# Kernel tuning notes

Measured on AMD Instinct MI355X. Metric: run time of the kernel, lower is better.

The kernel has to match this reference:

```python
import jax, jax.numpy as jnp
import numpy as np

NUM_CLASSES = 80        # dataset_train.num_classes() global in the original
NUM_SUPPORT_IMAGES = 5  # classification_batch[:5*num_anchors] in the original
ALPHA, GAMMA = 0.25, 2.0
STD = jnp.array([0.1, 0.1, 0.2, 0.2], dtype=jnp.float32)


def setup_inputs() -> dict:
    key = jax.random.key(0)
    k1, k2 = jax.random.split(key)
    n, tile = 320, 4.0
    A = n * n              # 102400 anchors
    B, G, z = 8, 16, 64
    gy, gx = jnp.meshgrid(jnp.arange(n, dtype=jnp.float32),
                          jnp.arange(n, dtype=jnp.float32), indexing='ij')
    x0 = gx.reshape(-1) * tile
    y0 = gy.reshape(-1) * tile
    anchor = jnp.stack([x0, y0, x0 + tile, y0 + tile], axis=1)  # [A,4] disjoint tiles
    anchors = anchor[None]                                       # [1,A,4]
    # GT boxes exactly equal distinct anchor tiles -> IoU 1 at match, 0 elsewhere.
    jj = jnp.arange(B)[:, None]
    gg = jnp.arange(G)[None, :]
    idx = (jj * 997 + gg * 3001) % A                             # distinct per image
    boxes = anchor[idx]                                          # [B,G,4]
    labels = jnp.broadcast_to((gg % 3).astype(jnp.float32), (B, G))
    annotations = jnp.concatenate([boxes, labels[..., None]], axis=-1)  # [B,G,5]
    classifications = jax.random.normal(k1, (B, A, z), dtype=jnp.float32)
    regressions = jax.random.normal(k2, (B, A, 4), dtype=jnp.float32)
    return {"classifications": classifications, "regressions": regressions,
            "anchors": anchors, "annotations": annotations}


def reference(classifications, regressions, anchors, annotations):
    B, A, z = classifications.shape
    anchor = anchors[0]                                   # [A,4]
    aw = anchor[:, 2] - anchor[:, 0]
    ah = anchor[:, 3] - anchor[:, 1]
    acx = anchor[:, 0] + 0.5 * aw
    acy = anchor[:, 1] + 0.5 * ah

    boxes = annotations[..., :4]                          # [B,G,4] (all valid, label != -1)
    labels = annotations[..., 4]                          # [B,G]

    # pairwise IoU  [B,A,G]  (calc_iou, vectorized over batch)
    area = (boxes[..., 2] - boxes[..., 0]) * (boxes[..., 3] - boxes[..., 1])  # [B,G]
    iw = jnp.minimum(anchor[None, :, None, 2], boxes[:, None, :, 2]) - \
         jnp.maximum(anchor[None, :, None, 0], boxes[:, None, :, 0])
    ih = jnp.minimum(anchor[None, :, None, 3], boxes[:, None, :, 3]) - \
         jnp.maximum(anchor[None, :, None, 1], boxes[:, None, :, 1])
    iw = jnp.maximum(iw, 0.0)
    ih = jnp.maximum(ih, 0.0)
    inter = iw * ih
    ua = jnp.maximum((aw * ah)[None, :, None] + area[:, None, :] - inter, 1e-8)
    iou = inter / ua
    iou_max = iou.max(axis=2)                             # [B,A]
    iou_arg = iou.argmax(axis=2)                          # [B,A]

    bidx = jnp.arange(B)[:, None]
    assigned_boxes = boxes[bidx, iou_arg]                 # [B,A,4]
    assigned_labels = labels[bidx, iou_arg]               # [B,A]

    pos = iou_max >= 0.5                                  # [B,A]
    targets_cls = jnp.where(iou_max < 0.4, float(NUM_CLASSES), -1.0)
    targets_cls = jnp.where(pos, assigned_labels, targets_cls)

    rgw = assigned_boxes[..., 2] - assigned_boxes[..., 0]
    rgh = assigned_boxes[..., 3] - assigned_boxes[..., 1]
    gcx = assigned_boxes[..., 0] + 0.5 * rgw              # centers use un-clamped w/h
    gcy = assigned_boxes[..., 1] + 0.5 * rgh
    gw = jnp.maximum(rgw, 1.0)
    gh = jnp.maximum(rgh, 1.0)
    tdx = (gcx - acx[None, :]) / aw[None, :]
    tdy = (gcy - acy[None, :]) / ah[None, :]
    tdw = jnp.log(gw / aw[None, :])
    tdh = jnp.log(gh / ah[None, :])
    t = jnp.stack([tdx, tdy, tdw, tdh], axis=-1) / STD    # [B,A,4]
    diff = jnp.abs(t - regressions)
    sl1 = jnp.where(diff <= 1.0 / 9.0, 0.5 * 9.0 * diff * diff, diff - 0.5 / 9.0)
    posf = pos.astype(sl1.dtype)
    npos = posf.sum(axis=1)                               # [B]
    reg_per_img = jnp.where(npos > 0,
                            (sl1 * posf[..., None]).sum(axis=(1, 2)) / jnp.maximum(4.0 * npos, 1.0),
                            0.0)
    reg_loss = reg_per_img.mean(keepdims=True)            # shape [1]

    # ---- prototypical focal classification loss ----
    emb = classifications.reshape(B * A, z)
    tgt = targets_cls.reshape(B * A)
    ns = NUM_SUPPORT_IMAGES * A
    emb_s, lab_s = emb[:ns], tgt[:ns]
    emb_q, lab_q = emb[ns:], tgt[ns:]
    valid = lab_q != -1.0                                 # query rows with assigned target

    # unique(labels_support) -- fixed {0,1,2,80} by input construction (assert len==4)
    classes = jnp.array([0.0, 1.0, 2.0, float(NUM_CLASSES)], dtype=emb.dtype)
    onehot = (lab_s[None, :] == classes[:, None]).astype(emb.dtype)   # [4,Ns]
    proto = (onehot @ emb_s) / jnp.maximum(onehot.sum(1, keepdims=True), 1.0)  # [4,z]

    dists = ((emb_q[:, None, :] - proto[None, :, :]) ** 2).sum(-1)    # [Nq,4]
    p_y = jax.nn.softmax(-dists, axis=1)
    tidx = jnp.clip(jnp.searchsorted(classes, lab_q), 0, classes.shape[0] - 1)
    prob = jnp.take_along_axis(p_y, tidx[:, None], axis=1)[:, 0]
    cls_term = -ALPHA * (1.0 - prob) ** GAMMA * jnp.log(prob)
    cls_term = jnp.where(valid, cls_term, 0.0)
    npq = (valid & (lab_q != float(NUM_CLASSES))).sum().astype(cls_term.dtype)
    cls_loss = cls_term.sum() / jnp.maximum(npq, 1.0)

    return cls_loss, reg_loss
```

## Files before the change

kernel.cpp:

```cpp
#include <hip/hip_runtime.h>

#define NB 8
#define NA 102400
#define NGRID 320
#define NG 16
#define NSUP 5
#define NQ 3
#define NCLSF 80.0f
#define NSLICE 8
#define SLS 264
#define WS_REG   (NSLICE * SLS)
#define WS_NPOS  (WS_REG + NB)
#define WS_CLS   (WS_NPOS + NB)
#define WS_NPQ   (WS_CLS + 4)
#define WS_FLOATS (WS_NPQ + 4)
#define BPI 400

__device__ __forceinline__ void anchor_of(int a, float& ax0, float& ay0,
                                          float& ax1, float& ay1) {
    int i = a / NGRID;
    int j = a - i * NGRID;
    ax0 = (float)j * 4.0f;
    ay0 = (float)i * 4.0f;
    ax1 = ax0 + 4.0f;
    ay1 = ay0 + 4.0f;
}

__device__ __forceinline__ void assign_anchor(const float* ann, int a,
                                              float& tgt, int& arg, float& iou_max) {
    float ax0, ay0, ax1, ay1;
    anchor_of(a, ax0, ay0, ax1, ay1);
    float aw = ax1 - ax0, ah = ay1 - ay0;
    float aarea = aw * ah;
    float best = -1.0f;
    int bi = 0;
    #pragma unroll
    for (int j = 0; j < NG; ++j) {
        float bx0 = ann[j * 5 + 0], by0 = ann[j * 5 + 1];
        float bx1 = ann[j * 5 + 2], by1 = ann[j * 5 + 3];
        float iw = fmaxf(fminf(ax1, bx1) - fmaxf(ax0, bx0), 0.0f);
        float ih = fmaxf(fminf(ay1, by1) - fmaxf(ay0, by0), 0.0f);
        float inter = iw * ih;
        float area = (bx1 - bx0) * (by1 - by0);
        float ua = fmaxf(aarea + area - inter, 1e-8f);
        float iou = inter / ua;
        if (iou > best) { best = iou; bi = j; }
    }
    iou_max = best;
    arg = bi;
    float lab = ann[bi * 5 + 4];
    tgt = (best >= 0.5f) ? lab : ((best < 0.4f) ? NCLSF : -1.0f);
}

__device__ __forceinline__ int code_of(float tgt) {
    int vld = (tgt != -1.0f) ? 4 : 0;
    int tix = (tgt == NCLSF) ? 3 : ((tgt == 2.0f) ? 2 : ((tgt == 1.0f) ? 1 : 0));
    return tix | vld;
}

__device__ __forceinline__ void reg_partial(const float* ann, int a, int arg, float im,
                                            const float* __restrict__ regressions,
                                            size_t row, float& sl1, float& posf) {
    sl1 = 0.0f; posf = 0.0f;
    if (im >= 0.5f) {
        posf = 1.0f;
        float ax0, ay0, ax1, ay1;
        anchor_of(a, ax0, ay0, ax1, ay1);
        float aw = ax1 - ax0, ah = ay1 - ay0;
        float acx = ax0 + 0.5f * aw, acy = ay0 + 0.5f * ah;
        const float* bb = ann + arg * 5;
        float rgw = bb[2] - bb[0], rgh = bb[3] - bb[1];
        float gcx = bb[0] + 0.5f * rgw, gcy = bb[1] + 0.5f * rgh;
        float gw = fmaxf(rgw, 1.0f), gh = fmaxf(rgh, 1.0f);
        float t0 = ((gcx - acx) / aw) / 0.1f;
        float t1 = ((gcy - acy) / ah) / 0.1f;
        float t2 = logf(gw / aw) / 0.2f;
        float t3 = logf(gh / ah) / 0.2f;
        const float4 rg4 = *reinterpret_cast<const float4*>(regressions + row * 4);
        float d0 = fabsf(t0 - rg4.x), d1 = fabsf(t1 - rg4.y);
        float d2 = fabsf(t2 - rg4.z), d3 = fabsf(t3 - rg4.w);
        sl1 += (d0 <= (1.0f/9.0f)) ? (4.5f * d0 * d0) : (d0 - 0.5f/9.0f);
        sl1 += (d1 <= (1.0f/9.0f)) ? (4.5f * d1 * d1) : (d1 - 0.5f/9.0f);
        sl1 += (d2 <= (1.0f/9.0f)) ? (4.5f * d2 * d2) : (d2 - 0.5f/9.0f);
        sl1 += (d3 <= (1.0f/9.0f)) ? (4.5f * d3 * d3) : (d3 - 0.5f/9.0f);
    }
}

__global__ __launch_bounds__(256, 3) void fl_proto(const float* __restrict__ annotations,
                                                   const float* __restrict__ cls,
                                                   const float* __restrict__ regressions,
                                                   float* __restrict__ ws) {
    __shared__ float s_ann[NG * 5];
    __shared__ float s_acc[256];
    __shared__ float s_sl1[4], s_np[4];
    __shared__ int   s_cnt[4];
    int b    = blockIdx.x / BPI;
    int cb   = blockIdx.x - b * BPI;
    int wid  = threadIdx.x >> 6;
    int lane = threadIdx.x & 63;
    int rg   = lane >> 4, li = lane & 15, zi = li * 4;
    int chunk = cb * 4 + wid;
    size_t row0 = (size_t)b * NA + (size_t)chunk * 64;

    float4 v[16];
    const float4* P = (const float4*)cls + (row0 + rg) * 16 + li;
    #pragma unroll
    for (int i = 0; i < 16; ++i) v[i] = P[(size_t)i * 64];

    if (threadIdx.x < NG * 5) s_ann[threadIdx.x] = annotations[b * NG * 5 + threadIdx.x];
    s_acc[threadIdx.x] = 0.0f;
    if (threadIdx.x < 4) s_cnt[threadIdx.x] = 0;
    __syncthreads();

    int a = chunk * 64 + lane;
    float tgt; int arg; float im;
    assign_anchor(s_ann, a, tgt, arg, im);
    int ci = code_of(tgt);

    float sl1, posf;
    reg_partial(s_ann, a, arg, im, regressions, row0 + lane, sl1, posf);
    #pragma unroll
    for (int s = 1; s < 64; s <<= 1) {
        sl1  += __shfl_xor(sl1, s, 64);
        posf += __shfl_xor(posf, s, 64);
    }
    if (lane == 0) { s_sl1[wid] = sl1; s_np[wid] = posf; }

    #pragma unroll
    for (int c = 0; c < 4; ++c) {
        unsigned long long m = __ballot(ci == (c | 4));
        if (lane == 0) atomicAdd(&s_cnt[c], (int)__popcll(m));
    }

    float acc[4][4] = {};
    #pragma unroll
    for (int i = 0; i < 16; ++i) {
        int cq = __shfl(ci, 4 * i + rg, 64);
        #pragma unroll
        for (int c = 0; c < 4; ++c) {
            float sel = (cq == (c | 4)) ? 1.0f : 0.0f;
            acc[c][0] = fmaf(sel, v[i].x, acc[c][0]);
            acc[c][1] = fmaf(sel, v[i].y, acc[c][1]);
            acc[c][2] = fmaf(sel, v[i].z, acc[c][2]);
            acc[c][3] = fmaf(sel, v[i].w, acc[c][3]);
        }
    }
    #pragma unroll
    for (int c = 0; c < 4; ++c) {
        #pragma unroll
        for (int k = 0; k < 4; ++k) {
            float vv = acc[c][k];
            vv += __shfl_xor(vv, 16, 64);
            vv += __shfl_xor(vv, 32, 64);
            if (lane < 16) atomicAdd(&s_acc[c * 64 + zi + k], vv);
        }
    }
    __syncthreads();
    int slice = blockIdx.x & (NSLICE - 1);
    atomicAdd(&ws[slice * SLS + threadIdx.x], s_acc[threadIdx.x]);
    if (threadIdx.x < 4 && s_cnt[threadIdx.x] > 0)
        atomicAdd(&ws[slice * SLS + 256 + threadIdx.x], (float)s_cnt[threadIdx.x]);
    if (threadIdx.x == 0) {
        atomicAdd(&ws[WS_REG + b],  s_sl1[0] + s_sl1[1] + s_sl1[2] + s_sl1[3]);
        atomicAdd(&ws[WS_NPOS + b], s_np[0] + s_np[1] + s_np[2] + s_np[3]);
    }
}

__global__ __launch_bounds__(256, 3) void fl_query(const float* __restrict__ annotations,
                                                   const float* __restrict__ cls,
                                                   const float* __restrict__ regressions,
                                                   float* __restrict__ ws) {
    __shared__ float s_ann[NG * 5];
    __shared__ float s_cls[4], s_npq[4], s_sl1[4], s_np[4];
    int qb   = blockIdx.x / BPI;
    int b    = NSUP + qb;
    int cb   = blockIdx.x - qb * BPI;
    int wid  = threadIdx.x >> 6;
    int lane = threadIdx.x & 63;
    int rg   = lane >> 4, li = lane & 15, zi = li * 4;
    int chunk = cb * 4 + wid;
    size_t row0 = (size_t)b * NA + (size_t)chunk * 64;

    float4 v[16];
    const float4* P = (const float4*)cls + (row0 + rg) * 16 + li;
    #pragma unroll
    for (int i = 0; i < 16; ++i) v[i] = P[(size_t)i * 64];

    if (threadIdx.x < NG * 5) s_ann[threadIdx.x] = annotations[b * NG * 5 + threadIdx.x];
    __syncthreads();

    float p[4][4], q[4];
    #pragma unroll
    for (int c = 0; c < 4; ++c) {
        float cv = 0.0f, s0 = 0.0f, s1 = 0.0f, s2 = 0.0f, s3 = 0.0f;
        #pragma unroll
        for (int s = 0; s < NSLICE; ++s) {
            cv += ws[s * SLS + 256 + c];
            const float4 u = *reinterpret_cast<const float4*>(&ws[s * SLS + c * 64 + zi]);
            s0 += u.x; s1 += u.y; s2 += u.z; s3 += u.w;
        }
        cv = fmaxf(cv, 1.0f);
        p[c][0] = s0 / cv; p[c][1] = s1 / cv; p[c][2] = s2 / cv; p[c][3] = s3 / cv;
        float qp = p[c][0]*p[c][0] + p[c][1]*p[c][1] + p[c][2]*p[c][2] + p[c][3]*p[c][3];
        qp += __shfl_xor(qp, 1, 64);
        qp += __shfl_xor(qp, 2, 64);
        qp += __shfl_xor(qp, 4, 64);
        qp += __shfl_xor(qp, 8, 64);
        q[c] = qp;
    }

    int a = chunk * 64 + lane;
    float tgt; int arg; float im;
    assign_anchor(s_ann, a, tgt, arg, im);
    int code = code_of(tgt);
    float sl1, posf;
    reg_partial(s_ann, a, arg, im, regressions, row0 + lane, sl1, posf);

    float clsAcc = 0.0f, npqAcc = 0.0f;
    #pragma unroll
    for (int i = 0; i < 16; ++i) {
        int cq = __shfl(code, 4 * i + rg, 64);
        float d0 = v[i].x*p[0][0] + v[i].y*p[0][1] + v[i].z*p[0][2] + v[i].w*p[0][3];
        float d1 = v[i].x*p[1][0] + v[i].y*p[1][1] + v[i].z*p[1][2] + v[i].w*p[1][3];
        float d2 = v[i].x*p[2][0] + v[i].y*p[2][1] + v[i].z*p[2][2] + v[i].w*p[2][3];
        float d3 = v[i].x*p[3][0] + v[i].y*p[3][1] + v[i].z*p[3][2] + v[i].w*p[3][3];
        #pragma unroll
        for (int s = 1; s < 16; s <<= 1) {
            d0 += __shfl_xor(d0, s, 64);
            d1 += __shfl_xor(d1, s, 64);
            d2 += __shfl_xor(d2, s, 64);
            d3 += __shfl_xor(d3, s, 64);
        }
        float l0 = 2.0f * d0 - q[0];
        float l1 = 2.0f * d1 - q[1];
        float l2 = 2.0f * d2 - q[2];
        float l3 = 2.0f * d3 - q[3];
        float m = fmaxf(fmaxf(l0, l1), fmaxf(l2, l3));
        float ex0 = expf(l0 - m), ex1 = expf(l1 - m);
        float ex2 = expf(l2 - m), ex3 = expf(l3 - m);
        float ssum = ex0 + ex1 + ex2 + ex3;
        int tq = cq & 3;
        float pnum = (tq == 0) ? ex0 : (tq == 1) ? ex1 : (tq == 2) ? ex2 : ex3;
        float prob = pnum / ssum;
        float om = 1.0f - prob;
        float term = -0.25f * om * om * logf(prob);
        if (li == 0 && (cq & 4)) {
            clsAcc += term;
            if (tq != 3) npqAcc += 1.0f;
        }
    }

    #pragma unroll
    for (int s = 1; s < 64; s <<= 1) {
        clsAcc += __shfl_xor(clsAcc, s, 64);
        npqAcc += __shfl_xor(npqAcc, s, 64);
        sl1    += __shfl_xor(sl1, s, 64);
        posf   += __shfl_xor(posf, s, 64);
    }
    if (lane == 0) { s_cls[wid] = clsAcc; s_npq[wid] = npqAcc; s_sl1[wid] = sl1; s_np[wid] = posf; }
    __syncthreads();
    if (threadIdx.x == 0) {
        int slice = blockIdx.x & 3;
        atomicAdd(&ws[WS_CLS + slice], s_cls[0] + s_cls[1] + s_cls[2] + s_cls[3]);
        atomicAdd(&ws[WS_NPQ + slice], s_npq[0] + s_npq[1] + s_npq[2] + s_npq[3]);
        atomicAdd(&ws[WS_REG + b],  s_sl1[0] + s_sl1[1] + s_sl1[2] + s_sl1[3]);
        atomicAdd(&ws[WS_NPOS + b], s_np[0] + s_np[1] + s_np[2] + s_np[3]);
    }
}

__global__ void fl_final(const float* __restrict__ ws, float* __restrict__ out) {
    if (threadIdx.x == 0 && blockIdx.x == 0) {
        float cs = ws[WS_CLS] + ws[WS_CLS+1] + ws[WS_CLS+2] + ws[WS_CLS+3];
        float nq = ws[WS_NPQ] + ws[WS_NPQ+1] + ws[WS_NPQ+2] + ws[WS_NPQ+3];
        float clsl = cs / fmaxf(nq, 1.0f);
        float rs = 0.0f;
        #pragma unroll
        for (int b = 0; b < NB; ++b) {
            float np_ = ws[WS_NPOS + b];
            float sv  = ws[WS_REG + b];
            rs += (np_ > 0.0f) ? (sv / fmaxf(4.0f * np_, 1.0f)) : 0.0f;
        }
        out[0] = clsl;
        out[1] = rs * 0.125f;
    }
}

extern "C" void kernel_launch(void* const* d_in, const int* in_sizes, int n_in,
                              void* d_out, int out_size, void* d_ws, size_t ws_size,
                              hipStream_t stream) {
    const float* classifications = (const float*)d_in[0];
    const float* regressions    = (const float*)d_in[1];
    const float* annotations    = (const float*)d_in[3];
    float* ws  = (float*)d_ws;
    float* out = (float*)d_out;

    hipMemsetAsync(d_ws, 0, WS_FLOATS * sizeof(float), stream);
    fl_proto<<<NSUP * BPI, 256, 0, stream>>>(annotations, classifications, regressions, ws);
    fl_query<<<NQ * BPI, 256, 0, stream>>>(annotations, classifications, regressions, ws);
    fl_final<<<1, 64, 0, stream>>>(ws, out);
}
```

Baseline: 127.1 us.

## Fuse proto, query and final kernels into one persistent kernel with grid barrier

```diff
diff --git a/kernel.cpp b/kernel.cpp
--- a/kernel.cpp
+++ b/kernel.cpp
@@ -13,8 +13,9 @@
 #define WS_NPOS  (WS_REG + NB)
 #define WS_CLS   (WS_NPOS + NB)
 #define WS_NPQ   (WS_CLS + 4)
-#define WS_FLOATS (WS_NPQ + 4)
-#define BPI 400
+#define WS_CNT   (WS_NPQ + 4)
+#define WS_FLOATS (WS_CNT + 2)
+#define NBLK 512
 
 __device__ __forceinline__ void anchor_of(int a, float& ax0, float& ay0,
                                           float& ax1, float& ay1) {
@@ -61,9 +62,8 @@
 __device__ __forceinline__ void reg_partial(const float* ann, int a, int arg, float im,
                                             const float* __restrict__ regressions,
                                             size_t row, float& sl1, float& posf) {
-    sl1 = 0.0f; posf = 0.0f;
     if (im >= 0.5f) {
-        posf = 1.0f;
+        posf += 1.0f;
         float ax0, ay0, ax1, ay1;
         anchor_of(a, ax0, ay0, ax1, ay1);
         float aw = ax1 - ax0, ah = ay1 - ay0;
@@ -86,108 +86,125 @@
     }
 }
 
-__global__ __launch_bounds__(256, 3) void fl_proto(const float* __restrict__ annotations,
+__global__ __launch_bounds__(256, 2) void fl_fused(const float* __restrict__ annotations,
                                                    const float* __restrict__ cls,
                                                    const float* __restrict__ regressions,
-                                                   float* __restrict__ ws) {
-    __shared__ float s_ann[NG * 5];
+                                                   float* __restrict__ ws,
+                                                   float* __restrict__ out) {
+    const int tid  = threadIdx.x;
+    const int lane = tid & 63, wid = tid >> 6;
+    const int gw   = blockIdx.x * 4 + wid;
+    const int rg   = lane >> 4, li = lane & 15, zi = li * 4;
+    unsigned* cnt = (unsigned*)(ws + WS_CNT);
+
     __shared__ float s_acc[256];
-    __shared__ float s_sl1[4], s_np[4];
-    __shared__ int   s_cnt[4];
-    int b    = blockIdx.x / BPI;
-    int cb   = blockIdx.x - b * BPI;
-    int wid  = threadIdx.x >> 6;
-    int lane = threadIdx.x & 63;
-    int rg   = lane >> 4, li = lane & 15, zi = li * 4;
-    int chunk = cb * 4 + wid;
-    size_t row0 = (size_t)b * NA + (size_t)chunk * 64;
-
-    float4 v[16];
-    const float4* P = (const float4*)cls + (row0 + rg) * 16 + li;
-    #pragma unroll
-    for (int i = 0; i < 16; ++i) v[i] = P[(size_t)i * 64];
-
-    if (threadIdx.x < NG * 5) s_ann[threadIdx.x] = annotations[b * NG * 5 + threadIdx.x];
-    s_acc[threadIdx.x] = 0.0f;
-    if (threadIdx.x < 4) s_cnt[threadIdx.x] = 0;
-    __syncthreads();
-
-    int a = chunk * 64 + lane;
-    float tgt; int arg; float im;
-    assign_anchor(s_ann, a, tgt, arg, im);
-    int ci = code_of(tgt);
-
-    float sl1, posf;
-    reg_partial(s_ann, a, arg, im, regressions, row0 + lane, sl1, posf);
+    __shared__ float s_cnt[4];
+    __shared__ float s_red[4][4];
+
+    s_acc[tid] = 0.0f;
+    if (tid < 4) s_cnt[tid] = 0.0f;
+    __syncthreads();
+
+    float sl1 = 0.0f, posf = 0.0f;
+    if (gw < 2000) {
+        const int b = gw / 400;
+        const float* ann = annotations + b * NG * 5;
+        float acc[4][4] = {};
+        float cc0 = 0.0f, cc1 = 0.0f, cc2 = 0.0f, cc3 = 0.0f;
+        for (int k = 0; k < 4; ++k) {
+            const int g   = gw * 4 + k;
+            const int cii = g - b * 1600;
+            const size_t row0 = (size_t)b * NA + (size_t)cii * 64;
+            const float4* P = (const float4*)cls + (row0 + rg) * 16 + li;
+            float4 v0[8];
+            #pragma unroll
+            for (int i = 0; i < 8; ++i) v0[i] = P[(size_t)i * 64];
+            const int a = cii * 64 + lane;
+            float tgt; int arg; float im;
+            assign_anchor(ann, a, tgt, arg, im);
+            const int ci = code_of(tgt);
+            reg_partial(ann, a, arg, im, regressions, row0 + lane, sl1, posf);
+            float4 v1[8];
+            #pragma unroll
+            for (int i = 0; i < 8; ++i) v1[i] = P[(size_t)(i + 8) * 64];
+            #pragma unroll
+            for (int i = 0; i < 8; ++i) {
+                const int cq = __shfl(ci, 4 * i + rg, 64);
+                #pragma unroll
+                for (int c = 0; c < 4; ++c) {
+                    const float sel = (cq == (c | 4)) ? 1.0f : 0.0f;
+                    acc[c][0] = fmaf(sel, v0[i].x, acc[c][0]);
+                    acc[c][1] = fmaf(sel, v0[i].y, acc[c][1]);
+                    acc[c][2] = fmaf(sel, v0[i].z, acc[c][2]);
+                    acc[c][3] = fmaf(sel, v0[i].w, acc[c][3]);
+                }
+            }
+            #pragma unroll
+            for (int i = 0; i < 8; ++i) {
+                const int cq = __shfl(ci, 4 * (i + 8) + rg, 64);
+                #pragma unroll
+                for (int c = 0; c < 4; ++c) {
+                    const float sel = (cq == (c | 4)) ? 1.0f : 0.0f;
+                    acc[c][0] = fmaf(sel, v1[i].x, acc[c][0]);
+                    acc[c][1] = fmaf(sel, v1[i].y, acc[c][1]);
+                    acc[c][2] = fmaf(sel, v1[i].z, acc[c][2]);
+                    acc[c][3] = fmaf(sel, v1[i].w, acc[c][3]);
+                }
+            }
+            cc0 += (float)__popcll(__ballot(ci == (0 | 4)));
+            cc1 += (float)__popcll(__ballot(ci == (1 | 4)));
+            cc2 += (float)__popcll(__ballot(ci == (2 | 4)));
+            cc3 += (float)__popcll(__ballot(ci == (3 | 4)));
+        }
+        #pragma unroll
+        for (int c = 0; c < 4; ++c) {
+            #pragma unroll
+            for (int k = 0; k < 4; ++k) {
+                float vv = acc[c][k];
+                vv += __shfl_xor(vv, 16, 64);
+                vv += __shfl_xor(vv, 32, 64);
+                if (lane < 16) atomicAdd(&s_acc[c * 64 + zi + k], vv);
+            }
+        }
+        if (lane == 0) {
+            atomicAdd(&s_cnt[0], cc0);
+            atomicAdd(&s_cnt[1], cc1);
+            atomicAdd(&s_cnt[2], cc2);
+            atomicAdd(&s_cnt[3], cc3);
+        }
+    }
     #pragma unroll
     for (int s = 1; s < 64; s <<= 1) {
         sl1  += __shfl_xor(sl1, s, 64);
         posf += __shfl_xor(posf, s, 64);
     }
-    if (lane == 0) { s_sl1[wid] = sl1; s_np[wid] = posf; }
-
-    #pragma unroll
-    for (int c = 0; c < 4; ++c) {
-        unsigned long long m = __ballot(ci == (c | 4));
-        if (lane == 0) atomicAdd(&s_cnt[c], (int)__popcll(m));
-    }
-
-    float acc[4][4] = {};
-    #pragma unroll
-    for (int i = 0; i < 16; ++i) {
-        int cq = __shfl(ci, 4 * i + rg, 64);
-        #pragma unroll
-        for (int c = 0; c < 4; ++c) {
-            float sel = (cq == (c | 4)) ? 1.0f : 0.0f;
-            acc[c][0] = fmaf(sel, v[i].x, acc[c][0]);
-            acc[c][1] = fmaf(sel, v[i].y, acc[c][1]);
-            acc[c][2] = fmaf(sel, v[i].z, acc[c][2]);
-            acc[c][3] = fmaf(sel, v[i].w, acc[c][3]);
-        }
-    }
-    #pragma unroll
-    for (int c = 0; c < 4; ++c) {
-        #pragma unroll
-        for (int k = 0; k < 4; ++k) {
-            float vv = acc[c][k];
-            vv += __shfl_xor(vv, 16, 64);
-            vv += __shfl_xor(vv, 32, 64);
-            if (lane < 16) atomicAdd(&s_acc[c * 64 + zi + k], vv);
-        }
-    }
-    __syncthreads();
-    int slice = blockIdx.x & (NSLICE - 1);
-    atomicAdd(&ws[slice * SLS + threadIdx.x], s_acc[threadIdx.x]);
-    if (threadIdx.x < 4 && s_cnt[threadIdx.x] > 0)
-        atomicAdd(&ws[slice * SLS + 256 + threadIdx.x], (float)s_cnt[threadIdx.x]);
-    if (threadIdx.x == 0) {
-        atomicAdd(&ws[WS_REG + b],  s_sl1[0] + s_sl1[1] + s_sl1[2] + s_sl1[3]);
-        atomicAdd(&ws[WS_NPOS + b], s_np[0] + s_np[1] + s_np[2] + s_np[3]);
-    }
-}
-
-__global__ __launch_bounds__(256, 3) void fl_query(const float* __restrict__ annotations,
-                                                   const float* __restrict__ cls,
-                                                   const float* __restrict__ regressions,
-                                                   float* __restrict__ ws) {
-    __shared__ float s_ann[NG * 5];
-    __shared__ float s_cls[4], s_npq[4], s_sl1[4], s_np[4];
-    int qb   = blockIdx.x / BPI;
-    int b    = NSUP + qb;
-    int cb   = blockIdx.x - qb * BPI;
-    int wid  = threadIdx.x >> 6;
-    int lane = threadIdx.x & 63;
-    int rg   = lane >> 4, li = lane & 15, zi = li * 4;
-    int chunk = cb * 4 + wid;
-    size_t row0 = (size_t)b * NA + (size_t)chunk * 64;
-
-    float4 v[16];
-    const float4* P = (const float4*)cls + (row0 + rg) * 16 + li;
-    #pragma unroll
-    for (int i = 0; i < 16; ++i) v[i] = P[(size_t)i * 64];
-
-    if (threadIdx.x < NG * 5) s_ann[threadIdx.x] = annotations[b * NG * 5 + threadIdx.x];
-    __syncthreads();
+    if (lane == 0) { s_red[wid][0] = sl1; s_red[wid][1] = posf; }
+    __syncthreads();
+
+    {
+        const int slice = blockIdx.x & (NSLICE - 1);
+        atomicAdd(&ws[slice * SLS + tid], s_acc[tid]);
+        if (tid < 4 && s_cnt[tid] > 0.0f)
+            atomicAdd(&ws[slice * SLS + 256 + tid], s_cnt[tid]);
+        if (tid == 0 && blockIdx.x < 500) {
+            const int b1 = (blockIdx.x * 4) / 400;
+            const float rs = s_red[0][0] + s_red[1][0] + s_red[2][0] + s_red[3][0];
+            const float ns = s_red[0][1] + s_red[1][1] + s_red[2][1] + s_red[3][1];
+            if (ns > 0.0f || rs != 0.0f) {
+                atomicAdd(&ws[WS_REG + b1],  rs);
+                atomicAdd(&ws[WS_NPOS + b1], ns);
+            }
+        }
+    }
+
+    __syncthreads();
+    if (tid == 0) {
+        __threadfence();
+        atomicAdd(&cnt[0], 1u);
+        while (atomicAdd(&cnt[0], 0u) < NBLK) __builtin_amdgcn_s_sleep(8);
+    }
+    __syncthreads();
+    __threadfence();
 
     float p[4][4], q[4];
     #pragma unroll
@@ -209,79 +226,103 @@
         q[c] = qp;
     }
 
-    int a = chunk * 64 + lane;
-    float tgt; int arg; float im;
-    assign_anchor(s_ann, a, tgt, arg, im);
-    int code = code_of(tgt);
-    float sl1, posf;
-    reg_partial(s_ann, a, arg, im, regressions, row0 + lane, sl1, posf);
-
-    float clsAcc = 0.0f, npqAcc = 0.0f;
-    #pragma unroll
-    for (int i = 0; i < 16; ++i) {
-        int cq = __shfl(code, 4 * i + rg, 64);
-        float d0 = v[i].x*p[0][0] + v[i].y*p[0][1] + v[i].z*p[0][2] + v[i].w*p[0][3];
-        float d1 = v[i].x*p[1][0] + v[i].y*p[1][1] + v[i].z*p[1][2] + v[i].w*p[1][3];
-        float d2 = v[i].x*p[2][0] + v[i].y*p[2][1] + v[i].z*p[2][2] + v[i].w*p[2][3];
-        float d3 = v[i].x*p[3][0] + v[i].y*p[3][1] + v[i].z*p[3][2] + v[i].w*p[3][3];
-        #pragma unroll
-        for (int s = 1; s < 16; s <<= 1) {
-            d0 += __shfl_xor(d0, s, 64);
-            d1 += __shfl_xor(d1, s, 64);
-            d2 += __shfl_xor(d2, s, 64);
-            d3 += __shfl_xor(d3, s, 64);
-        }
-        float l0 = 2.0f * d0 - q[0];
-        float l1 = 2.0f * d1 - q[1];
-        float l2 = 2.0f * d2 - q[2];
-        float l3 = 2.0f * d3 - q[3];
-        float m = fmaxf(fmaxf(l0, l1), fmaxf(l2, l3));
-        float ex0 = expf(l0 - m), ex1 = expf(l1 - m);
-        float ex2 = expf(l2 - m), ex3 = expf(l3 - m);
-        float ssum = ex0 + ex1 + ex2 + ex3;
-        int tq = cq & 3;
-        float pnum = (tq == 0) ? ex0 : (tq == 1) ? ex1 : (tq == 2) ? ex2 : ex3;
-        float prob = pnum / ssum;
-        float om = 1.0f - prob;
-        float term = -0.25f * om * om * logf(prob);
-        if (li == 0 && (cq & 4)) {
-            clsAcc += term;
-            if (tq != 3) npqAcc += 1.0f;
-        }
-    }
-
+    float clsAcc = 0.0f, npqAcc = 0.0f, sl1q = 0.0f, posq = 0.0f;
+    if (gw < 1200) {
+        const int qb = gw / 400;
+        const int b  = NSUP + qb;
+        const float* ann = annotations + b * NG * 5;
+        for (int k = 0; k < 4; ++k) {
+            const int g   = gw * 4 + k;
+            const int cii = g - qb * 1600;
+            const size_t row0 = (size_t)b * NA + (size_t)cii * 64;
+            const float4* P = (const float4*)cls + (row0 + rg) * 16 + li;
+            float4 v0[8];
+            #pragma unroll
+            for (int i = 0; i < 8; ++i) v0[i] = P[(size_t)i * 64];
+            const int a = cii * 64 + lane;
+            float tgt; int arg; float im;
+            assign_anchor(ann, a, tgt, arg, im);
+            const int code = code_of(tgt);
+            reg_partial(ann, a, arg, im, regressions, row0 + lane, sl1q, posq);
+            float4 v1[8];
+            #pragma unroll
+            for (int i = 0; i < 8; ++i) v1[i] = P[(size_t)(i + 8) * 64];
+            #pragma unroll
+            for (int i = 0; i < 16; ++i) {
+                const float4 e = (i < 8) ? v0[i & 7] : v1[i & 7];
+                const int cq = __shfl(code, 4 * i + rg, 64);
+                float d0 = e.x*p[0][0] + e.y*p[0][1] + e.z*p[0][2] + e.w*p[0][3];
+                float d1 = e.x*p[1][0] + e.y*p[1][1] + e.z*p[1][2] + e.w*p[1][3];
+                float d2 = e.x*p[2][0] + e.y*p[2][1] + e.z*p[2][2] + e.w*p[2][3];
+                float d3 = e.x*p[3][0] + e.y*p[3][1] + e.z*p[3][2] + e.w*p[3][3];
+                #pragma unroll
+                for (int s = 1; s < 16; s <<= 1) {
+                    d0 += __shfl_xor(d0, s, 64);
+                    d1 += __shfl_xor(d1, s, 64);
+                    d2 += __shfl_xor(d2, s, 64);
+                    d3 += __shfl_xor(d3, s, 64);
+                }
+                const float l0 = 2.0f * d0 - q[0];
+                const float l1 = 2.0f * d1 - q[1];
+                const float l2 = 2.0f * d2 - q[2];
+                const float l3 = 2.0f * d3 - q[3];
+                const float m = fmaxf(fmaxf(l0, l1), fmaxf(l2, l3));
+                const float ex0 = expf(l0 - m), ex1 = expf(l1 - m);
+                const float ex2 = expf(l2 - m), ex3 = expf(l3 - m);
+                const float ssum = ex0 + ex1 + ex2 + ex3;
+                const int tq = cq & 3;
+                const float pnum = (tq == 0) ? ex0 : (tq == 1) ? ex1 : (tq == 2) ? ex2 : ex3;
+                const float prob = pnum / ssum;
+                const float om = 1.0f - prob;
+                const float term = -0.25f * om * om * logf(prob);
+                if (li == 0 && (cq & 4)) {
+                    clsAcc += term;
+                    if (tq != 3) npqAcc += 1.0f;
+                }
+            }
+        }
+    }
     #pragma unroll
     for (int s = 1; s < 64; s <<= 1) {
         clsAcc += __shfl_xor(clsAcc, s, 64);
         npqAcc += __shfl_xor(npqAcc, s, 64);
-        sl1    += __shfl_xor(sl1, s, 64);
-        posf   += __shfl_xor(posf, s, 64);
-    }
-    if (lane == 0) { s_cls[wid] = clsAcc; s_npq[wid] = npqAcc; s_sl1[wid] = sl1; s_np[wid] = posf; }
-    __syncthreads();
-    if (threadIdx.x == 0) {
-        int slice = blockIdx.x & 3;
-        atomicAdd(&ws[WS_CLS + slice], s_cls[0] + s_cls[1] + s_cls[2] + s_cls[3]);
-        atomicAdd(&ws[WS_NPQ + slice], s_npq[0] + s_npq[1] + s_npq[2] + s_npq[3]);
-        atomicAdd(&ws[WS_REG + b],  s_sl1[0] + s_sl1[1] + s_sl1[2] + s_sl1[3]);
-        atomicAdd(&ws[WS_NPOS + b], s_np[0] + s_np[1] + s_np[2] + s_np[3]);
-    }
-}
-
-__global__ void fl_final(const float* __restrict__ ws, float* __restrict__ out) {
-    if (threadIdx.x == 0 && blockIdx.x == 0) {
-        float cs = ws[WS_CLS] + ws[WS_CLS+1] + ws[WS_CLS+2] + ws[WS_CLS+3];
-        float nq = ws[WS_NPQ] + ws[WS_NPQ+1] + ws[WS_NPQ+2] + ws[WS_NPQ+3];
-        float clsl = cs / fmaxf(nq, 1.0f);
-        float rs = 0.0f;
-        #pragma unroll
-        for (int b = 0; b < NB; ++b) {
-            float np_ = ws[WS_NPOS + b];
-            float sv  = ws[WS_REG + b];
-            rs += (np_ > 0.0f) ? (sv / fmaxf(4.0f * np_, 1.0f)) : 0.0f;
-        }
-        out[0] = clsl;
-        out[1] = rs * 0.125f;
+        sl1q   += __shfl_xor(sl1q, s, 64);
+        posq   += __shfl_xor(posq, s, 64);
+    }
+    __syncthreads();
+    if (lane == 0) {
+        s_red[wid][0] = clsAcc; s_red[wid][1] = npqAcc;
+        s_red[wid][2] = sl1q;   s_red[wid][3] = posq;
+    }
+    __syncthreads();
+    if (tid == 0 && blockIdx.x < 300) {
+        const int slice = blockIdx.x & 3;
+        atomicAdd(&ws[WS_CLS + slice], s_red[0][0] + s_red[1][0] + s_red[2][0] + s_red[3][0]);
+        atomicAdd(&ws[WS_NPQ + slice], s_red[0][1] + s_red[1][1] + s_red[2][1] + s_red[3][1]);
+        const int b2 = NSUP + (blockIdx.x * 4) / 400;
+        atomicAdd(&ws[WS_REG + b2],  s_red[0][2] + s_red[1][2] + s_red[2][2] + s_red[3][2]);
+        atomicAdd(&ws[WS_NPOS + b2], s_red[0][3] + s_red[1][3] + s_red[2][3] + s_red[3][3]);
+    }
+
+    __syncthreads();
+    if (tid == 0) {
+        __threadfence();
+        atomicAdd(&cnt[1], 1u);
+        if (blockIdx.x == 0) {
+            while (atomicAdd(&cnt[1], 0u) < NBLK) __builtin_amdgcn_s_sleep(8);
+            __threadfence();
+            const float cs = ws[WS_CLS] + ws[WS_CLS+1] + ws[WS_CLS+2] + ws[WS_CLS+3];
+            const float nq = ws[WS_NPQ] + ws[WS_NPQ+1] + ws[WS_NPQ+2] + ws[WS_NPQ+3];
+            float rs = 0.0f;
+            #pragma unroll
+            for (int b = 0; b < NB; ++b) {
+                const float np_ = ws[WS_NPOS + b];
+                const float sv  = ws[WS_REG + b];
+                rs += (np_ > 0.0f) ? (sv / fmaxf(4.0f * np_, 1.0f)) : 0.0f;
+            }
+            out[0] = cs / fmaxf(nq, 1.0f);
+            out[1] = rs * 0.125f;
+        }
     }
 }
 
@@ -295,7 +336,5 @@
     float* out = (float*)d_out;
 
     hipMemsetAsync(d_ws, 0, WS_FLOATS * sizeof(float), stream);
-    fl_proto<<<NSUP * BPI, 256, 0, stream>>>(annotations, classifications, regressions, ws);
-    fl_query<<<NQ * BPI, 256, 0, stream>>>(annotations, classifications, regressions, ws);
-    fl_final<<<1, 64, 0, stream>>>(ws, out);
-}
+    fl_fused<<<NBLK, 256, 0, stream>>>(annotations, classifications, regressions, ws, out);
+}
```

New measurement: 163.6 us. 1.29x slower.
